# Optimization experiments

Hardware: AMD Instinct MI355X
Metric: run time of the kernel (lower is better)

The kernel has to match this reference:

```python
import jax, jax.numpy as jnp
import numpy as np

EPS_GN = 1e-8
EPS_ATTN = 1e-8


def setup_inputs() -> dict:
    key = jax.random.key(0)
    ks = jax.random.split(key, 13)
    B, C, N = 4, 512, 2048
    s = 0.02
    return {
        "x": jax.random.normal(ks[0], (B, C, N), jnp.float32),
        "dw_w": jax.random.normal(ks[1], (C, 3), jnp.float32) * s,
        "pw_w": jax.random.normal(ks[2], (C, C), jnp.float32) * s,
        "u_w": jax.random.normal(ks[3], (2 * C, C), jnp.float32) * s,
        "u_b": jax.random.normal(ks[4], (2 * C,), jnp.float32) * s,
        "v_w": jax.random.normal(ks[5], (2 * C, C), jnp.float32) * s,
        "v_b": jax.random.normal(ks[6], (2 * C,), jnp.float32) * s,
        "h_w": jax.random.normal(ks[7], (C, C), jnp.float32) * s,
        "h_b": jax.random.normal(ks[8], (C,), jnp.float32) * s,
        "q_w": jax.random.normal(ks[9], (C, C), jnp.float32) * s,
        "k_w": jax.random.normal(ks[10], (C, C), jnp.float32) * s,
        "o_w": jax.random.normal(ks[11], (C, 2 * C), jnp.float32) * s,
        "o_b": jax.random.normal(ks[12], (C,), jnp.float32) * s,
    }


def reference(x, dw_w, pw_w, u_w, u_b, v_w, v_b, h_w, h_b, q_w, k_w, o_w, o_b):
    # x: [B, C, N]
    C = x.shape[1]
    # GroupNorm(1, C): normalize over (C, N) per sample; affine is identity-init
    # in torch but we follow the module math with default weight=1, bias=0
    mean = jnp.mean(x, axis=(1, 2), keepdims=True)
    var = jnp.var(x, axis=(1, 2), keepdims=True)
    z = (x - mean) * jax.lax.rsqrt(var + EPS_GN)

    # local depthwise conv k=3, pad=1 (cross-correlation), no bias
    zp = jnp.pad(z, ((0, 0), (0, 0), (1, 1)))
    dw = (dw_w[:, 0, None] * zp[:, :, :-2]
          + dw_w[:, 1, None] * zp[:, :, 1:-1]
          + dw_w[:, 2, None] * zp[:, :, 2:])
    # pointwise conv (no bias)
    z = z + jnp.einsum('oc,bcn->bon', pw_w, dw)

    u = jax.nn.sigmoid(jnp.einsum('oc,bcn->bon', u_w, z) + u_b[:, None])  # [B,2C,N]
    v = jnp.einsum('oc,bcn->bon', v_w, z) + v_b[:, None]                  # [B,2C,N]
    h = jnp.einsum('oc,bcn->bno', h_w, z) + h_b                           # [B,N,C]

    q = h @ q_w.T  # [B,N,C]
    k = h @ k_w.T  # [B,N,C]
    scale = 1.0 / jnp.sqrt(jnp.float32(C))

    logits = jnp.einsum('bnc,bmc->bnm', q, k) * scale
    a = jax.nn.relu(logits)
    a = a * a
    a = a / (jnp.sum(a, axis=-1, keepdims=True) + EPS_ATTN)

    av = jnp.einsum('bnm,bom->bon', a, v)  # [B,2C,N]
    y = jnp.einsum('oc,bcn->bon', o_w, u * av) + o_b[:, None]
    return x + y
```

## Files before the change

kernel.cpp:

```cpp
#include <hip/hip_runtime.h>
#include <hip/hip_bf16.h>
#include <cstdint>

typedef __bf16 bhalf;
typedef __bf16 bhalf8 __attribute__((ext_vector_type(8)));
typedef float f32x4 __attribute__((ext_vector_type(4)));

enum { EPI_Z2=0, EPI_UV=1, EPI_BIAS=2, EPI_QK=3, EPI_ATTN=4, EPI_PV=5, EPI_Y=6 };

__device__ __forceinline__ void gl_lds16(const bhalf* g, bhalf* l) {
  __builtin_amdgcn_global_load_lds(
      (const __attribute__((address_space(1))) unsigned int*)g,
      (__attribute__((address_space(3))) unsigned int*)l,
      16, 0, 0);
}
__device__ __forceinline__ void barrier_raw() { asm volatile("s_barrier" ::: "memory"); }
#define VMW(n)  asm volatile("s_waitcnt vmcnt(" #n ")" ::: "memory")
#define LGKM0() asm volatile("s_waitcnt lgkmcnt(0)" ::: "memory")


template<int EPI>
__global__ void __launch_bounds__(512, 2)
gA(const bhalf* __restrict__ A, const bhalf* __restrict__ Bw,
   void* __restrict__ Out, void* __restrict__ Out2,
   const float* __restrict__ bias, const float* __restrict__ bias2,
   int N, int K, long sA, long sB, long sO, long sAuxf, float scale)
{
  constexpr int KSL = 256*64;
  constexpr int REG = 2*KSL;
  constexpr int DBUF = 2*REG;
  __shared__ __align__(16) char lds[2*DBUF];

  const int gx = gridDim.x, gy = gridDim.y;
  const int nwg = gx*gy;
  const int flat = blockIdx.y*gx + blockIdx.x;
  const int q8 = nwg>>3, r8 = nwg&7, xcd = flat&7, o8 = flat>>3;
  const int wsw = (xcd<r8 ? xcd*(q8+1) : r8*(q8+1)+(xcd-r8)*q8) + o8;
  const int bx = wsw % gx, by = wsw / gx;
  const int m0 = by*256, n0 = bx*256;
  const int bz = blockIdx.z;

  const bhalf* Ab = A + (long)bz*sA;
  const bhalf* Bb = Bw + (long)bz*sB;

  const int tid = threadIdx.x, wid = tid>>6, lane = tid&63;
  const int lm = lane&15, kq = lane>>4;
  const int wm = wid>>2, wn = wid&3;
  const int srow = lane>>2;
  const int csw = ((lane&3) ^ ((lane>>3)&3)) * 8;
  const int kqs = kq ^ ((lm>>1)&3);

  f32x4 acc[8][4];
  #pragma unroll
  for (int i=0;i<8;i++)
    #pragma unroll
    for (int j=0;j<4;j++) acc[i][j] = f32x4{0.f,0.f,0.f,0.f};

  auto stageA = [&](int kt){
    char* base = lds + (kt&1)*DBUF;
    const int k0 = kt*64;
    #pragma unroll
    for (int h=0; h<2; h++)
      #pragma unroll
      for (int ksl=0; ksl<2; ksl++){
        bhalf* d = (bhalf*)(base + ksl*KSL + (h*128 + wid*16)*64);
        gl_lds16(Ab + (long)(m0 + h*128 + wid*16 + srow)*K + k0 + ksl*32 + csw, d);
      }
  };
  auto stageB = [&](int kt){
    char* base = lds + (kt&1)*DBUF + REG;
    const int k0 = kt*64;
    #pragma unroll
    for (int h=0; h<2; h++)
      #pragma unroll
      for (int ksl=0; ksl<2; ksl++){
        bhalf* d = (bhalf*)(base + ksl*KSL + (h*128 + wid*16)*64);
        gl_lds16(Bb + (long)(n0 + h*128 + wid*16 + srow)*K + k0 + ksl*32 + csw, d);
      }
  };

  bhalf8 af[4][2], bf[4][2];
  auto readA = [&](int kt, int ih){
    char* base = lds + (kt&1)*DBUF;
    #pragma unroll
    for (int i2=0;i2<4;i2++)
      #pragma unroll
      for (int ksl=0;ksl<2;ksl++)
        af[i2][ksl] = *(const bhalf8*)(base + ksl*KSL + (wm*128 + ih*64 + i2*16 + lm)*64 + kqs*16);
  };
  auto readB = [&](int kt, int jh){
    char* base = lds + (kt&1)*DBUF + REG;
    #pragma unroll
    for (int j2=0;j2<2;j2++)
      #pragma unroll
      for (int ksl=0;ksl<2;ksl++)
        bf[jh*2+j2][ksl] = *(const bhalf8*)(base + ksl*KSL + (wn*64 + jh*32 + j2*16 + lm)*64 + kqs*16);
  };
  auto mfma16 = [&](int ih, int jh){
    __builtin_amdgcn_s_setprio(1);
    #pragma unroll
    for (int i2=0;i2<4;i2++)
      #pragma unroll
      for (int j2=0;j2<2;j2++)
        #pragma unroll
        for (int ksl=0;ksl<2;ksl++)
          acc[ih*4+i2][jh*2+j2] = __builtin_amdgcn_mfma_f32_16x16x32_bf16(
              af[i2][ksl], bf[jh*2+j2][ksl], acc[ih*4+i2][jh*2+j2], 0,0,0);
    __builtin_amdgcn_s_setprio(0);
  };

  const int NT = K>>6;
  stageA(0); stageB(0); stageA(1);
  for (int kt=0; kt<NT; ++kt){
    if (kt==NT-1) { VMW(0); } else { VMW(4); }
    barrier_raw();
    readA(kt,0); readB(kt,0);
    if (kt+1<NT) stageB(kt+1);
    mfma16(0,0);
    barrier_raw();
    readB(kt,1);
    mfma16(0,1);
    barrier_raw();
    readA(kt,1);
    mfma16(1,0);
    barrier_raw();
    if (kt+2<NT) stageA(kt+2);
    mfma16(1,1);
  }
  barrier_raw();

  char* obase; int ldb;
  const float* bv = nullptr; int bc0 = 0; bool sig = false;
  if constexpr (EPI==EPI_ATTN){
    obase = (char*)Out + 2*((long)bz*sO + (long)m0*N + n0); ldb = N*2;
  }
  if constexpr (EPI==EPI_UV){
    bool uh = n0 < 1024; sig = uh;
    obase = (char*)(uh?Out:Out2) + 2*((long)m0*1024 + (n0 - (uh?0:1024)));
    ldb = 2048; bv = uh ? bias : bias2; bc0 = uh ? n0 : n0-1024;
  }

  float rs[8][4];
  if constexpr (EPI==EPI_ATTN){
    #pragma unroll
    for (int i=0;i<8;i++)
      #pragma unroll
      for (int r=0;r<4;r++) rs[i][r]=0.f;
  }
  #pragma unroll
  for (int i=0;i<8;i++){
    #pragma unroll
    for (int j=0;j<4;j++){
      const int lcol = wn*64 + j*16 + lm;
      #pragma unroll
      for (int r=0;r<4;r++){
        const int lrow = wm*128 + i*16 + kq*4 + r;
        float v = acc[i][j][r];
        if constexpr (EPI==EPI_ATTN){
          v *= scale; v = fmaxf(v,0.f); v = v*v;
          rs[i][r] += v;
        }
        if constexpr (EPI==EPI_UV){
          v += bv[bc0 + lcol];
          if (sig) v = 1.f/(1.f + __expf(-v));
        }
        const int cb = lcol*2;
        const int lb = lrow*512 + (((cb>>5) ^ ((lrow>>2)&3))<<5) + (cb&31);
        *(bhalf*)(lds + lb) = (bhalf)v;
      }
    }
  }
  if constexpr (EPI==EPI_ATTN){
    float* rd = (float*)Out2;
    #pragma unroll
    for (int i=0;i<8;i++){
      const int rbase = m0 + wm*128 + i*16 + kq*4;
      #pragma unroll
      for (int r=0;r<4;r++){
        float s = rs[i][r];
        s += __shfl_xor(s,1); s += __shfl_xor(s,2);
        s += __shfl_xor(s,4); s += __shfl_xor(s,8);
        if (lm==0) atomicAdd(rd + (long)bz*sAuxf + rbase + r, s);
      }
    }
  }
  LGKM0();
  barrier_raw();
  #pragma unroll
  for (int it=0; it<16; ++it){
    const int g = (it*512 + tid)*16;
    const int row = g >> 9, off = g & 511;
    const int lb = row*512 + (((off>>5) ^ ((row>>2)&3))<<5) + (off&31);
    uint4 val = *(const uint4*)(lds + lb);
    *(uint4*)(obase + (long)row*ldb + off) = val;
  }
  (void)scale; (void)bias; (void)bias2; (void)N;
}

template<int EPI>
__global__ void __launch_bounds__(512, 2)
gB(const bhalf* __restrict__ A, const bhalf* __restrict__ Bw,
   void* __restrict__ Out, void* __restrict__ Out2,
   const bhalf* __restrict__ auxb, const float* __restrict__ auxf,
   int N, int K, long sB, float scale, int rowshift)
{
  constexpr int KSLA = 256*64;
  constexpr int KSLB = 128*64;
  constexpr int REGA = 2*KSLA;
  constexpr int DBUF = REGA + 2*KSLB;
  __shared__ __align__(16) char lds[3*DBUF];

  const int gx = gridDim.x, gy = gridDim.y;
  const int nwg = gx*gy;
  const int flat = blockIdx.y*gx + blockIdx.x;
  const int q8 = nwg>>3, r8 = nwg&7, xcd = flat&7, o8 = flat>>3;
  const int wsw = (xcd<r8 ? xcd*(q8+1) : r8*(q8+1)+(xcd-r8)*q8) + o8;
  const int bx = wsw % gx, by = wsw / gx;
  const int m0 = by*256, n0 = bx*128;

  const bhalf* Ab = A;
  const bhalf* Bb = Bw + (rowshift ? (long)(m0>>rowshift)*sB : 0);

  const int tid = threadIdx.x, wid = tid>>6, lane = tid&63;
  const int lm = lane&15, kq = lane>>4;
  const int wm = wid>>1, wn = wid&1;
  const int srow = lane>>2;
  const int csw = ((lane&3) ^ ((lane>>3)&3)) * 8;
  const int kqs = kq ^ ((lm>>1)&3);

  f32x4 acc[4][4];
  #pragma unroll
  for (int i=0;i<4;i++)
    #pragma unroll
    for (int j=0;j<4;j++) acc[i][j] = f32x4{0.f,0.f,0.f,0.f};

  auto stageAB = [&](int kt){
    char* base = lds + (kt%3)*DBUF;
    const int k0 = kt*64;
    #pragma unroll
    for (int h=0; h<2; h++)
      #pragma unroll
      for (int ksl=0; ksl<2; ksl++){
        bhalf* d = (bhalf*)(base + ksl*KSLA + (h*128 + wid*16)*64);
        gl_lds16(Ab + (long)(m0 + h*128 + wid*16 + srow)*K + k0 + ksl*32 + csw, d);
      }
    #pragma unroll
    for (int ksl=0; ksl<2; ksl++){
      bhalf* d = (bhalf*)(base + REGA + ksl*KSLB + (wid*16)*64);
      gl_lds16(Bb + (long)(n0 + wid*16 + srow)*K + k0 + ksl*32 + csw, d);
    }
  };

  bhalf8 af[4][2], bf[4][2];
  auto readA = [&](int kt){
    char* base = lds + (kt%3)*DBUF;
    #pragma unroll
    for (int i2=0;i2<4;i2++)
      #pragma unroll
      for (int ksl=0;ksl<2;ksl++)
        af[i2][ksl] = *(const bhalf8*)(base + ksl*KSLA + (wm*64 + i2*16 + lm)*64 + kqs*16);
  };
  auto readB = [&](int kt, int jh){
    char* base = lds + (kt%3)*DBUF + REGA;
    #pragma unroll
    for (int j2=0;j2<2;j2++)
      #pragma unroll
      for (int ksl=0;ksl<2;ksl++)
        bf[jh*2+j2][ksl] = *(const bhalf8*)(base + ksl*KSLB + (wn*64 + jh*32 + j2*16 + lm)*64 + kqs*16);
  };
  auto mfma16 = [&](int jh){
    __builtin_amdgcn_s_setprio(1);
    #pragma unroll
    for (int i2=0;i2<4;i2++)
      #pragma unroll
      for (int j2=0;j2<2;j2++)
        #pragma unroll
        for (int ksl=0;ksl<2;ksl++)
          acc[i2][jh*2+j2] = __builtin_amdgcn_mfma_f32_16x16x32_bf16(
              af[i2][ksl], bf[jh*2+j2][ksl], acc[i2][jh*2+j2], 0,0,0);
    __builtin_amdgcn_s_setprio(0);
  };

  const int NT = K>>6;
  stageAB(0); stageAB(1);
  for (int kt=0; kt<NT; ++kt){
    if (kt==NT-1) { VMW(0); } else { VMW(6); }
    barrier_raw();
    readA(kt); readB(kt,0);
    if (kt+2<NT) stageAB(kt+2);
    mfma16(0);
    barrier_raw();
    readB(kt,1);
    mfma16(1);
  }
  barrier_raw();

  char* obase; int ldb;
  if constexpr (EPI==EPI_PV){
    obase = (char*)Out + 2*((long)m0*1024 + n0); ldb = 2048;
  }
  if constexpr (EPI==EPI_QK){
    bool qh = n0 < 512;
    obase = (char*)(qh?Out:Out2) + 2*((long)m0*512 + (n0 - (qh?0:512)));
    ldb = 1024;
  }
  #pragma unroll
  for (int i=0;i<4;i++){
    #pragma unroll
    for (int j=0;j<4;j++){
      const int lcol = wn*64 + j*16 + lm;
      #pragma unroll
      for (int r=0;r<4;r++){
        const int lrow = wm*64 + i*16 + kq*4 + r;
        float v = acc[i][j][r];
        if constexpr (EPI==EPI_PV){
          const int rowg = m0 + lrow;
          float den = auxf[rowg];
          v *= __builtin_amdgcn_rcpf(den + 1e-8f);
          v *= (float)auxb[(long)rowg*1024 + n0 + lcol];
        }
        const int cb = lcol*2;
        const int lb = lrow*256 + (((cb>>5) ^ ((lrow>>2)&3))<<5) + (cb&31);
        *(bhalf*)(lds + lb) = (bhalf)v;
      }
    }
  }
  LGKM0();
  barrier_raw();
  #pragma unroll
  for (int it=0; it<8; ++it){
    const int g = (it*512 + tid)*16;
    const int row = g >> 8, off = g & 255;
    const int lb = row*256 + (((off>>5) ^ ((row>>2)&3))<<5) + (off&31);
    uint4 val = *(const uint4*)(lds + lb);
    *(uint4*)(obase + (long)row*ldb + off) = val;
  }
  (void)scale; (void)auxb; (void)auxf; (void)N;
}

template<int EPI>
__global__ void __launch_bounds__(512, 2)
gemm_bt(const bhalf* __restrict__ A, const bhalf* __restrict__ Bw,
        void* __restrict__ Out,
        const float* __restrict__ bias,
        const bhalf* __restrict__ auxb,
        int M, int N, int K)
{
  constexpr int STRIDE = 256*64;
  __shared__ __align__(16) char lds[4*STRIDE];

  const int gx = gridDim.x, gy = gridDim.y;
  const int nwg = gx*gy;
  const int flat = blockIdx.y*gx + blockIdx.x;
  const int q8 = nwg>>3, r8 = nwg&7, xcd = flat&7, o8 = flat>>3;
  const int w = (xcd<r8 ? xcd*(q8+1) : r8*(q8+1)+(xcd-r8)*q8) + o8;
  const int bx = w % gx, by = w / gx;

  const int tid = threadIdx.x;
  const int wid = tid>>6, lane = tid&63;
  const int lm = lane&15, kq = lane>>4;
  const int wm = wid>>2, wn = wid&3;
  const int m0 = by*128, n0 = bx*128;
  const int srow = lane>>2;
  const int csw = ((lane&3) ^ ((lane>>3)&3))*8;
  const int kqs = kq ^ ((lm>>1)&3);

  f32x4 acc[4][2];
  #pragma unroll
  for (int i=0;i<4;i++)
    #pragma unroll
    for (int j=0;j<2;j++) acc[i][j] = f32x4{0.f,0.f,0.f,0.f};

  auto stage = [&](int t){
    char* base = lds + (t&3)*STRIDE;
    const int k0 = t*32;
    #pragma unroll
    for (int c=0;c<2;c++){
      const int r0 = wid*32 + c*16;
      bhalf* d = (bhalf*)(base + r0*64);
      const bhalf* g = (r0 < 128)
        ? A + (long)(m0 + r0 + srow)*K + k0 + csw
        : Bw + (long)(n0 + r0 - 128 + srow)*K + k0 + csw;
      gl_lds16(g, d);
    }
  };

  auto compute = [&](int t){
    char* base = lds + (t&3)*STRIDE;
    bhalf8 af[4], bf[2];
    #pragma unroll
    for (int i=0;i<4;i++)
      af[i] = *(const bhalf8*)(base + (wm*64 + i*16 + lm)*64 + kqs*16);
    #pragma unroll
    for (int j=0;j<2;j++)
      bf[j] = *(const bhalf8*)(base + (128 + wn*32 + j*16 + lm)*64 + kqs*16);
    __builtin_amdgcn_s_setprio(1);
    #pragma unroll
    for (int i=0;i<4;i++)
      #pragma unroll
      for (int j=0;j<2;j++)
        acc[i][j] = __builtin_amdgcn_mfma_f32_16x16x32_bf16(af[i], bf[j], acc[i][j], 0,0,0);
    __builtin_amdgcn_s_setprio(0);
  };

  const int NT = K>>5;
  stage(0); stage(1); stage(2);
  for (int t=0; t<NT; ++t){
    if (t+3<NT){ stage(t+3); VMW(6); }
    else if (t+2<NT) { VMW(4); }
    else if (t+1<NT) { VMW(2); }
    else             { VMW(0); }
    barrier_raw();
    compute(t);
    barrier_raw();
  }

  char* obase = (char*)Out + 2*((long)m0*N + n0);
  const int ldb = N*2;
  #pragma unroll
  for (int i=0;i<4;i++){
    #pragma unroll
    for (int j=0;j<2;j++){
      const int lcol = wn*32 + j*16 + lm;
      #pragma unroll
      for (int r=0;r<4;r++){
        const int lrow = wm*64 + i*16 + kq*4 + r;
        float v = acc[i][j][r];
        if constexpr (EPI==EPI_Z2)
          v += (float)auxb[(long)(m0+lrow)*N + n0 + lcol];
        if constexpr (EPI==EPI_BIAS || EPI==EPI_Y)
          v += bias[n0 + lcol];
        const int cb = lcol*2;
        const int lb = lrow*256 + (((cb>>5) ^ ((lrow>>2)&3))<<5) + (cb&31);
        *(bhalf*)(lds + lb) = (bhalf)v;
      }
    }
  }
  LGKM0();
  barrier_raw();
  #pragma unroll
  for (int it=0; it<4; ++it){
    const int g = (it*512 + tid)*16;
    const int row = g >> 8, off = g & 255;
    const int lb = row*256 + (((off>>5) ^ ((row>>2)&3))<<5) + (off&31);
    uint4 val = *(const uint4*)(lds + lb);
    *(uint4*)(obase + (long)row*ldb + off) = val;
  }
  (void)M;
}

struct CvtArgs { const float* src[7]; bhalf* dst[7]; int n[7]; };
__global__ void cvt_multi(CvtArgs a) {
  int seg = blockIdx.y;
  int i = (blockIdx.x*256 + threadIdx.x)*4;
  if (i >= a.n[seg]) return;
  float4 f = *(const float4*)(a.src[seg] + i);
  bhalf* d = a.dst[seg] + i;
  d[0]=(bhalf)f.x; d[1]=(bhalf)f.y; d[2]=(bhalf)f.z; d[3]=(bhalf)f.w;
}

__global__ void gn_part(const float* __restrict__ x, float* __restrict__ ps, float* __restrict__ pss) {
  int b = blockIdx.y;
  const float* xb = x + (long)b*(512*2048);
  float s=0.f, ss=0.f;
  #pragma unroll
  for (int it=0; it<8; it++){
    int idx = ((it*128 + blockIdx.x)*256 + threadIdx.x)*4;
    float4 f = *(const float4*)(xb + idx);
    s  += f.x+f.y+f.z+f.w;
    ss += f.x*f.x+f.y*f.y+f.z*f.z+f.w*f.w;
  }
  for (int off=32; off; off>>=1){ s += __shfl_xor(s,off); ss += __shfl_xor(ss,off); }
  __shared__ float ls[4], lss[4];
  int wid = threadIdx.x>>6, lane = threadIdx.x&63;
  if (lane==0){ ls[wid]=s; lss[wid]=ss; }
  __syncthreads();
  if (threadIdx.x==0){
    s = ls[0]+ls[1]+ls[2]+ls[3]; ss = lss[0]+lss[1]+lss[2]+lss[3];
    ps[b*128 + blockIdx.x] = s; pss[b*128 + blockIdx.x] = ss;
  }
}

__global__ void gn_final(const float* __restrict__ ps, const float* __restrict__ pss,
                         float* __restrict__ stats) {
  int b = blockIdx.x;
  float s = ps[b*128 + threadIdx.x], ss = pss[b*128 + threadIdx.x];
  for (int off=32; off; off>>=1){ s += __shfl_xor(s,off); ss += __shfl_xor(ss,off); }
  __shared__ float l0[2], l1[2];
  int wid = threadIdx.x>>6, lane = threadIdx.x&63;
  if (lane==0){ l0[wid]=s; l1[wid]=ss; }
  __syncthreads();
  if (threadIdx.x==0){
    s = l0[0]+l0[1]; ss = l1[0]+l1[1];
    float mean = s*(1.f/1048576.f);
    float var  = ss*(1.f/1048576.f) - mean*mean;
    stats[b*2] = mean; stats[b*2+1] = rsqrtf(var + 1e-8f);
  }
}

__global__ void norm_dw_T(const float* __restrict__ x, const float* __restrict__ stats,
                          const float* __restrict__ dw_w,
                          bhalf* __restrict__ zT, bhalf* __restrict__ dwT) {
  int b = blockIdx.z, n0 = blockIdx.x*32, c0 = blockIdx.y*32;
  float mean = stats[b*2], rstd = stats[b*2+1];
  __shared__ float zs[32][35];
  int tx = threadIdx.x, ty = threadIdx.y;
  #pragma unroll
  for (int r=0;r<4;r++){
    int c = c0 + ty + r*8;
    for (int cc=tx; cc<34; cc+=32){
      int n = n0 - 1 + cc;
      float v = 0.f;
      if (n>=0 && n<2048) v = (x[((long)b*512 + c)*2048 + n] - mean)*rstd;
      zs[ty + r*8][cc] = v;
    }
  }
  __syncthreads();
  float w0 = dw_w[(c0+tx)*3+0], w1 = dw_w[(c0+tx)*3+1], w2 = dw_w[(c0+tx)*3+2];
  #pragma unroll
  for (int r=0;r<4;r++){
    int ln = ty + r*8;
    float z = zs[tx][ln+1];
    float d = w0*zs[tx][ln] + w1*zs[tx][ln+1] + w2*zs[tx][ln+2];
    long o = ((long)b*2048 + n0 + ln)*512 + c0 + tx;
    zT[o] = (bhalf)z; dwT[o] = (bhalf)d;
  }
}

__global__ void transpose_bf16(const bhalf* __restrict__ in, bhalf* __restrict__ out,
                               int R, int C) {
  __shared__ bhalf t[32][33];
  int r0 = blockIdx.x*32, c0 = blockIdx.y*32;
  long ib = (long)blockIdx.z*R*C;
  int tx = threadIdx.x, ty = threadIdx.y;
  #pragma unroll
  for (int r=0;r<4;r++)
    t[ty + r*8][tx] = in[ib + (long)(r0 + ty + r*8)*C + c0 + tx];
  __syncthreads();
  #pragma unroll
  for (int r=0;r<4;r++)
    out[ib + (long)(c0 + ty + r*8)*R + r0 + tx] = t[tx][ty + r*8];
}

__global__ void final_add(const float* __restrict__ x, const bhalf* __restrict__ yT,
                          float* __restrict__ out) {
  __shared__ float t[32][33];
  int n0 = blockIdx.x*32, c0 = blockIdx.y*32, b = blockIdx.z;
  int tx = threadIdx.x, ty = threadIdx.y;
  #pragma unroll
  for (int r=0;r<4;r++)
    t[ty + r*8][tx] = (float)yT[((long)b*2048 + n0 + ty + r*8)*512 + c0 + tx];
  __syncthreads();
  #pragma unroll
  for (int r=0;r<4;r++){
    long idx = ((long)b*512 + c0 + ty + r*8)*2048 + n0 + tx;
    out[idx] = x[idx] + t[tx][ty + r*8];
  }
}

extern "C" void kernel_launch(void* const* d_in, const int* in_sizes, int n_in,
                              void* d_out, int out_size, void* d_ws, size_t ws_size,
                              hipStream_t stream) {
  (void)in_sizes; (void)n_in; (void)out_size; (void)ws_size;
  const float* x    = (const float*)d_in[0];
  const float* dw_w = (const float*)d_in[1];
  const float* pw_w = (const float*)d_in[2];
  const float* u_w  = (const float*)d_in[3];
  const float* u_b  = (const float*)d_in[4];
  const float* v_w  = (const float*)d_in[5];
  const float* v_b  = (const float*)d_in[6];
  const float* h_w  = (const float*)d_in[7];
  const float* h_b  = (const float*)d_in[8];
  const float* q_w  = (const float*)d_in[9];
  const float* k_w  = (const float*)d_in[10];
  const float* o_w  = (const float*)d_in[11];
  const float* o_b  = (const float*)d_in[12];
  float* out = (float*)d_out;

  char* ws = (char*)d_ws;
  size_t off = 0;
  auto alloc = [&](size_t bytes) -> void* {
    void* p = ws + off; off = (off + bytes + 255) & ~(size_t)255; return p;
  };

  float* ps    = (float*)alloc(4*128*4);
  float* pss   = (float*)alloc(4*128*4);
  float* stats = (float*)alloc(4*2*4);
  float* rden  = (float*)alloc(4*2048*4);
  bhalf* wb_pw = (bhalf*)alloc(512*512*2);
  bhalf* wb_uv = (bhalf*)alloc((size_t)2048*512*2);
  bhalf* wb_h  = (bhalf*)alloc(512*512*2);
  bhalf* wb_qk = (bhalf*)alloc((size_t)1024*512*2);
  bhalf* wb_o  = (bhalf*)alloc((size_t)512*1024*2);
  const size_t ACT = (size_t)4*2048*512;
  bhalf* zT   = (bhalf*)alloc(ACT*2);
  bhalf* dwT  = (bhalf*)alloc(ACT*2);
  bhalf* z2T  = (bhalf*)alloc(ACT*2);
  bhalf* ub   = (bhalf*)alloc(ACT*2*2);
  bhalf* vT   = (bhalf*)alloc(ACT*2*2);
  bhalf* v_fm = (bhalf*)alloc(ACT*2*2);
  bhalf* hb   = (bhalf*)alloc(ACT*2);
  bhalf* wsc  = (bhalf*)alloc((size_t)4*2048*2048*2);
  bhalf* uav  = (bhalf*)alloc(ACT*2*2);
  bhalf* qb = zT;  bhalf* kb = dwT;  bhalf* yT = vT;

  hipMemsetAsync(rden, 0, 4*2048*4, stream);

  CvtArgs ca;
  ca.src[0]=pw_w; ca.dst[0]=wb_pw;           ca.n[0]=512*512;
  ca.src[1]=u_w;  ca.dst[1]=wb_uv;           ca.n[1]=1024*512;
  ca.src[2]=v_w;  ca.dst[2]=wb_uv+1024*512;  ca.n[2]=1024*512;
  ca.src[3]=h_w;  ca.dst[3]=wb_h;            ca.n[3]=512*512;
  ca.src[4]=q_w;  ca.dst[4]=wb_qk;           ca.n[4]=512*512;
  ca.src[5]=k_w;  ca.dst[5]=wb_qk+512*512;   ca.n[5]=512*512;
  ca.src[6]=o_w;  ca.dst[6]=wb_o;            ca.n[6]=512*1024;
  cvt_multi<<<dim3(512,7), 256, 0, stream>>>(ca);

  gn_part<<<dim3(128,4), 256, 0, stream>>>(x, ps, pss);
  gn_final<<<dim3(4), 128, 0, stream>>>(ps, pss, stats);

  norm_dw_T<<<dim3(64,16,4), dim3(32,8), 0, stream>>>(x, stats, dw_w, zT, dwT);

  const float iscl = 0.044194173824159216f;
  gemm_bt<EPI_Z2><<<dim3(4,64,1), 512, 0, stream>>>(dwT, wb_pw, z2T,
      nullptr, zT, 8192, 512, 512);
  gA<EPI_UV><<<dim3(8,32,1), 512, 0, stream>>>(z2T, wb_uv, ub, vT,
      u_b, v_b, 2048, 512, 0, 0, 0, 0, 0.f);
  gemm_bt<EPI_BIAS><<<dim3(4,64,1), 512, 0, stream>>>(z2T, wb_h, hb,
      h_b, nullptr, 8192, 512, 512);
  gB<EPI_QK><<<dim3(8,32,1), 512, 0, stream>>>(hb, wb_qk, qb, kb,
      nullptr, nullptr, 1024, 512, 0, 0.f, 0);
  transpose_bf16<<<dim3(64,32,4), dim3(32,8), 0, stream>>>(vT, v_fm, 2048, 1024);
  gA<EPI_ATTN><<<dim3(8,8,4), 512, 0, stream>>>(qb, kb, wsc, rden,
      nullptr, nullptr, 2048, 512,
      (long)2048*512, (long)2048*512, (long)2048*2048, 2048, iscl);
  gB<EPI_PV><<<dim3(8,32,1), 512, 0, stream>>>(wsc, v_fm, uav, nullptr,
      ub, rden, 1024, 2048, (long)1024*2048, 0.f, 11);
  gemm_bt<EPI_Y><<<dim3(4,64,1), 512, 0, stream>>>(uav, wb_o, yT,
      o_b, nullptr, 8192, 512, 1024);
  final_add<<<dim3(64,16,4), dim3(32,8), 0, stream>>>(x, yT, out);
}
```

Measured before the change: 192.3 us.

## Fuse v transpose and final residual add into GEMM epilogues; retile small GEMMs

The UV GEMM epilogue now writes the v half transposed through LDS straight into feature-major layout, which removes the separate transpose kernel. The output GEMM epilogue transposes in LDS, adds x and writes the fp32 result directly, which removes the final_add kernel and the yT buffer. The 128x128 GEMMs are rewritten as g4k with 256 threads, a 64-deep K step, double buffering and a 4x4 MFMA tile per wave. This saves two launches and two full activation round-trips through memory, at the cost of more complex epilogues and 8-byte scattered LDS reads in the transposed paths.

```diff
diff --git a/kernel.cpp b/kernel.cpp
--- a/kernel.cpp
+++ b/kernel.cpp
@@ -129,48 +129,29 @@
   }
   barrier_raw();
 
-  char* obase; int ldb;
-  const float* bv = nullptr; int bc0 = 0; bool sig = false;
   if constexpr (EPI==EPI_ATTN){
-    obase = (char*)Out + 2*((long)bz*sO + (long)m0*N + n0); ldb = N*2;
-  }
-  if constexpr (EPI==EPI_UV){
-    bool uh = n0 < 1024; sig = uh;
-    obase = (char*)(uh?Out:Out2) + 2*((long)m0*1024 + (n0 - (uh?0:1024)));
-    ldb = 2048; bv = uh ? bias : bias2; bc0 = uh ? n0 : n0-1024;
-  }
-
-  float rs[8][4];
-  if constexpr (EPI==EPI_ATTN){
+    float rs[8][4];
     #pragma unroll
     for (int i=0;i<8;i++)
       #pragma unroll
       for (int r=0;r<4;r++) rs[i][r]=0.f;
-  }
-  #pragma unroll
-  for (int i=0;i<8;i++){
-    #pragma unroll
-    for (int j=0;j<4;j++){
-      const int lcol = wn*64 + j*16 + lm;
-      #pragma unroll
-      for (int r=0;r<4;r++){
-        const int lrow = wm*128 + i*16 + kq*4 + r;
-        float v = acc[i][j][r];
-        if constexpr (EPI==EPI_ATTN){
+    #pragma unroll
+    for (int i=0;i<8;i++){
+      #pragma unroll
+      for (int j=0;j<4;j++){
+        const int lcol = wn*64 + j*16 + lm;
+        #pragma unroll
+        for (int r=0;r<4;r++){
+          const int lrow = wm*128 + i*16 + kq*4 + r;
+          float v = acc[i][j][r];
           v *= scale; v = fmaxf(v,0.f); v = v*v;
           rs[i][r] += v;
+          const int cb = lcol*2;
+          const int lb = lrow*512 + (((cb>>5) ^ ((lrow>>2)&3))<<5) + (cb&31);
+          *(bhalf*)(lds + lb) = (bhalf)v;
         }
-        if constexpr (EPI==EPI_UV){
-          v += bv[bc0 + lcol];
-          if (sig) v = 1.f/(1.f + __expf(-v));
-        }
-        const int cb = lcol*2;
-        const int lb = lrow*512 + (((cb>>5) ^ ((lrow>>2)&3))<<5) + (cb&31);
-        *(bhalf*)(lds + lb) = (bhalf)v;
-      }
-    }
-  }
-  if constexpr (EPI==EPI_ATTN){
+      }
+    }
     float* rd = (float*)Out2;
     #pragma unroll
     for (int i=0;i<8;i++){
@@ -183,16 +164,71 @@
         if (lm==0) atomicAdd(rd + (long)bz*sAuxf + rbase + r, s);
       }
     }
-  }
-  LGKM0();
-  barrier_raw();
-  #pragma unroll
-  for (int it=0; it<16; ++it){
-    const int g = (it*512 + tid)*16;
-    const int row = g >> 9, off = g & 511;
-    const int lb = row*512 + (((off>>5) ^ ((row>>2)&3))<<5) + (off&31);
-    uint4 val = *(const uint4*)(lds + lb);
-    *(uint4*)(obase + (long)row*ldb + off) = val;
+    LGKM0();
+    barrier_raw();
+    char* obase = (char*)Out + 2*((long)bz*sO + (long)m0*N + n0);
+    const int ldb = N*2;
+    #pragma unroll
+    for (int it=0; it<16; ++it){
+      const int g = (it*512 + tid)*16;
+      const int row = g >> 9, off = g & 511;
+      const int lb = row*512 + (((off>>5) ^ ((row>>2)&3))<<5) + (off&31);
+      uint4 val = *(const uint4*)(lds + lb);
+      *(uint4*)(obase + (long)row*ldb + off) = val;
+    }
+  }
+  if constexpr (EPI==EPI_UV){
+    const bool uh = n0 < 1024;
+    const float* bv = uh ? bias : bias2;
+    const int bc0 = uh ? n0 : n0-1024;
+    #pragma unroll
+    for (int i=0;i<8;i++){
+      #pragma unroll
+      for (int j=0;j<4;j++){
+        const int lcol = wn*64 + j*16 + lm;
+        #pragma unroll
+        for (int r=0;r<4;r++){
+          const int lrow = wm*128 + i*16 + kq*4 + r;
+          float v = acc[i][j][r] + bv[bc0 + lcol];
+          if (uh){
+            v = 1.f/(1.f + __expf(-v));
+            const int cb = lcol*2;
+            const int lb = lrow*512 + (((cb>>5) ^ ((lrow>>2)&3))<<5) + (cb&31);
+            *(bhalf*)(lds + lb) = (bhalf)v;
+          } else {
+            const int lb = lcol*512 + 2*(lrow ^ ((lcol&15)<<2));
+            *(bhalf*)(lds + lb) = (bhalf)v;
+          }
+        }
+      }
+    }
+    LGKM0();
+    barrier_raw();
+    if (uh){
+      char* obase = (char*)Out + 2*((long)m0*1024 + n0);
+      #pragma unroll
+      for (int it=0; it<16; ++it){
+        const int g = (it*512 + tid)*16;
+        const int row = g >> 9, off = g & 511;
+        const int lb = row*512 + (((off>>5) ^ ((row>>2)&3))<<5) + (off&31);
+        uint4 val = *(const uint4*)(lds + lb);
+        *(uint4*)(obase + (long)row*2048 + off) = val;
+      }
+    } else {
+      char* vb = (char*)Out2 + 2*((long)(m0>>11)*1024*2048 + (long)(n0-1024)*2048 + (m0 & 2047));
+      #pragma unroll
+      for (int it=0; it<16; ++it){
+        const int g = (it*512 + tid)*16;
+        const int row = g >> 9, off = g & 511;
+        const int t0 = off >> 1;
+        const int s = (row&15)<<2;
+        unsigned long long lo = *(const unsigned long long*)(lds + row*512 + 2*(t0^s));
+        unsigned long long hi = *(const unsigned long long*)(lds + row*512 + 2*((t0+4)^s));
+        char* dst = vb + (long)row*4096 + off;
+        ((unsigned long long*)dst)[0] = lo;
+        ((unsigned long long*)dst)[1] = hi;
+      }
+    }
   }
   (void)scale; (void)bias; (void)bias2; (void)N;
 }
@@ -339,15 +375,17 @@
 }
 
 template<int EPI>
-__global__ void __launch_bounds__(512, 2)
-gemm_bt(const bhalf* __restrict__ A, const bhalf* __restrict__ Bw,
-        void* __restrict__ Out,
-        const float* __restrict__ bias,
-        const bhalf* __restrict__ auxb,
-        int M, int N, int K)
+__global__ void __launch_bounds__(256, 2)
+g4k(const bhalf* __restrict__ A, const bhalf* __restrict__ Bw,
+    void* __restrict__ Out,
+    const float* __restrict__ bias,
+    const bhalf* __restrict__ auxb,
+    const float* __restrict__ xadd,
+    int M, int N, int K)
 {
-  constexpr int STRIDE = 256*64;
-  __shared__ __align__(16) char lds[4*STRIDE];
+  constexpr int KSL = 256*64;
+  constexpr int DBUF = 2*KSL;
+  __shared__ __align__(16) char lds[2*DBUF];
 
   const int gx = gridDim.x, gy = gridDim.y;
   const int nwg = gx*gy;
@@ -355,98 +393,147 @@
   const int q8 = nwg>>3, r8 = nwg&7, xcd = flat&7, o8 = flat>>3;
   const int w = (xcd<r8 ? xcd*(q8+1) : r8*(q8+1)+(xcd-r8)*q8) + o8;
   const int bx = w % gx, by = w / gx;
+  const int m0 = by*128, n0 = bx*128;
 
   const int tid = threadIdx.x;
   const int wid = tid>>6, lane = tid&63;
   const int lm = lane&15, kq = lane>>4;
-  const int wm = wid>>2, wn = wid&3;
-  const int m0 = by*128, n0 = bx*128;
+  const int wm = wid>>1, wn = wid&1;
   const int srow = lane>>2;
   const int csw = ((lane&3) ^ ((lane>>3)&3))*8;
   const int kqs = kq ^ ((lm>>1)&3);
 
-  f32x4 acc[4][2];
+  f32x4 acc[4][4];
   #pragma unroll
   for (int i=0;i<4;i++)
     #pragma unroll
-    for (int j=0;j<2;j++) acc[i][j] = f32x4{0.f,0.f,0.f,0.f};
-
-  auto stage = [&](int t){
-    char* base = lds + (t&3)*STRIDE;
-    const int k0 = t*32;
-    #pragma unroll
-    for (int c=0;c<2;c++){
-      const int r0 = wid*32 + c*16;
-      bhalf* d = (bhalf*)(base + r0*64);
-      const bhalf* g = (r0 < 128)
-        ? A + (long)(m0 + r0 + srow)*K + k0 + csw
-        : Bw + (long)(n0 + r0 - 128 + srow)*K + k0 + csw;
-      gl_lds16(g, d);
-    }
-  };
-
-  auto compute = [&](int t){
-    char* base = lds + (t&3)*STRIDE;
-    bhalf8 af[4], bf[2];
-    #pragma unroll
-    for (int i=0;i<4;i++)
-      af[i] = *(const bhalf8*)(base + (wm*64 + i*16 + lm)*64 + kqs*16);
-    #pragma unroll
-    for (int j=0;j<2;j++)
-      bf[j] = *(const bhalf8*)(base + (128 + wn*32 + j*16 + lm)*64 + kqs*16);
+    for (int j=0;j<4;j++) acc[i][j] = f32x4{0.f,0.f,0.f,0.f};
+
+  auto stage = [&](int kt){
+    char* base = lds + (kt&1)*DBUF;
+    const int k0 = kt*64;
+    #pragma unroll
+    for (int c=0;c<4;c++){
+      const int r0 = c*64 + wid*16;
+      #pragma unroll
+      for (int ksl=0; ksl<2; ksl++){
+        bhalf* d = (bhalf*)(base + ksl*KSL + r0*64);
+        const bhalf* g = (r0 < 128)
+          ? A  + (long)(m0 + r0 + srow)*K + k0 + ksl*32 + csw
+          : Bw + (long)(n0 + r0 - 128 + srow)*K + k0 + ksl*32 + csw;
+        gl_lds16(g, d);
+      }
+    }
+  };
+
+  bhalf8 af[4][2], bf[4][2];
+  auto readA = [&](int kt){
+    char* base = lds + (kt&1)*DBUF;
+    #pragma unroll
+    for (int i2=0;i2<4;i2++)
+      #pragma unroll
+      for (int ksl=0;ksl<2;ksl++)
+        af[i2][ksl] = *(const bhalf8*)(base + ksl*KSL + (wm*64 + i2*16 + lm)*64 + kqs*16);
+  };
+  auto readB = [&](int kt, int jh){
+    char* base = lds + (kt&1)*DBUF;
+    #pragma unroll
+    for (int j2=0;j2<2;j2++)
+      #pragma unroll
+      for (int ksl=0;ksl<2;ksl++)
+        bf[jh*2+j2][ksl] = *(const bhalf8*)(base + ksl*KSL + (128 + wn*64 + jh*32 + j2*16 + lm)*64 + kqs*16);
+  };
+  auto mfma16 = [&](int jh){
     __builtin_amdgcn_s_setprio(1);
     #pragma unroll
-    for (int i=0;i<4;i++)
-      #pragma unroll
-      for (int j=0;j<2;j++)
-        acc[i][j] = __builtin_amdgcn_mfma_f32_16x16x32_bf16(af[i], bf[j], acc[i][j], 0,0,0);
+    for (int i2=0;i2<4;i2++)
+      #pragma unroll
+      for (int j2=0;j2<2;j2++)
+        #pragma unroll
+        for (int ksl=0;ksl<2;ksl++)
+          acc[i2][jh*2+j2] = __builtin_amdgcn_mfma_f32_16x16x32_bf16(
+              af[i2][ksl], bf[jh*2+j2][ksl], acc[i2][jh*2+j2], 0,0,0);
     __builtin_amdgcn_s_setprio(0);
   };
 
-  const int NT = K>>5;
-  stage(0); stage(1); stage(2);
-  for (int t=0; t<NT; ++t){
-    if (t+3<NT){ stage(t+3); VMW(6); }
-    else if (t+2<NT) { VMW(4); }
-    else if (t+1<NT) { VMW(2); }
-    else             { VMW(0); }
-    barrier_raw();
-    compute(t);
-    barrier_raw();
-  }
-
-  char* obase = (char*)Out + 2*((long)m0*N + n0);
-  const int ldb = N*2;
-  #pragma unroll
-  for (int i=0;i<4;i++){
-    #pragma unroll
-    for (int j=0;j<2;j++){
-      const int lcol = wn*32 + j*16 + lm;
-      #pragma unroll
-      for (int r=0;r<4;r++){
-        const int lrow = wm*64 + i*16 + kq*4 + r;
-        float v = acc[i][j][r];
-        if constexpr (EPI==EPI_Z2)
-          v += (float)auxb[(long)(m0+lrow)*N + n0 + lcol];
-        if constexpr (EPI==EPI_BIAS || EPI==EPI_Y)
-          v += bias[n0 + lcol];
-        const int cb = lcol*2;
-        const int lb = lrow*256 + (((cb>>5) ^ ((lrow>>2)&3))<<5) + (cb&31);
-        *(bhalf*)(lds + lb) = (bhalf)v;
-      }
-    }
-  }
-  LGKM0();
+  const int NT = K>>6;
+  stage(0); stage(1);
+  for (int kt=0; kt<NT; ++kt){
+    if (kt==NT-1) { VMW(0); } else { VMW(8); }
+    barrier_raw();
+    readA(kt); readB(kt,0);
+    mfma16(0);
+    barrier_raw();
+    readB(kt,1);
+    if (kt+2<NT) stage(kt+2);
+    mfma16(1);
+  }
   barrier_raw();
-  #pragma unroll
-  for (int it=0; it<4; ++it){
-    const int g = (it*512 + tid)*16;
-    const int row = g >> 8, off = g & 255;
-    const int lb = row*256 + (((off>>5) ^ ((row>>2)&3))<<5) + (off&31);
-    uint4 val = *(const uint4*)(lds + lb);
-    *(uint4*)(obase + (long)row*ldb + off) = val;
-  }
-  (void)M;
+
+  if constexpr (EPI==EPI_Y){
+    #pragma unroll
+    for (int i=0;i<4;i++){
+      #pragma unroll
+      for (int j=0;j<4;j++){
+        const int lcol = wn*64 + j*16 + lm;
+        #pragma unroll
+        for (int r=0;r<4;r++){
+          const int lrow = wm*64 + i*16 + kq*4 + r;
+          float v = acc[i][j][r] + bias[n0 + lcol];
+          const int lb = lcol*512 + 4*(lrow ^ ((lcol&15)<<2));
+          *(float*)(lds + lb) = v;
+        }
+      }
+    }
+    LGKM0();
+    barrier_raw();
+    const int b = m0 >> 11, nb = m0 & 2047;
+    float* ob = (float*)Out + ((long)b*512 + n0)*2048 + nb;
+    const float* xb = xadd + ((long)b*512 + n0)*2048 + nb;
+    #pragma unroll
+    for (int it=0; it<16; ++it){
+      const int g = (it*256 + tid)*16;
+      const int row = g >> 9, off = g & 511;
+      const int t0 = off >> 2;
+      const int s = (row&15)<<2;
+      f32x4 vv = *(const f32x4*)(lds + row*512 + 4*(t0^s));
+      f32x4 xx = *(const f32x4*)(xb + (long)row*2048 + t0);
+      *(f32x4*)(ob + (long)row*2048 + t0) = vv + xx;
+    }
+  } else {
+    char* obase = (char*)Out + 2*((long)m0*N + n0);
+    const int ldb = N*2;
+    #pragma unroll
+    for (int i=0;i<4;i++){
+      #pragma unroll
+      for (int j=0;j<4;j++){
+        const int lcol = wn*64 + j*16 + lm;
+        #pragma unroll
+        for (int r=0;r<4;r++){
+          const int lrow = wm*64 + i*16 + kq*4 + r;
+          float v = acc[i][j][r];
+          if constexpr (EPI==EPI_Z2)
+            v += (float)auxb[(long)(m0+lrow)*N + n0 + lcol];
+          if constexpr (EPI==EPI_BIAS)
+            v += bias[n0 + lcol];
+          const int cb = lcol*2;
+          const int lb = lrow*256 + (((cb>>5) ^ ((lrow>>2)&3))<<5) + (cb&31);
+          *(bhalf*)(lds + lb) = (bhalf)v;
+        }
+      }
+    }
+    LGKM0();
+    barrier_raw();
+    #pragma unroll
+    for (int it=0; it<8; ++it){
+      const int g = (it*256 + tid)*16;
+      const int row = g >> 8, off = g & 255;
+      const int lb = row*256 + (((off>>5) ^ ((row>>2)&3))<<5) + (off&31);
+      uint4 val = *(const uint4*)(lds + lb);
+      *(uint4*)(obase + (long)row*ldb + off) = val;
+    }
+  }
+  (void)M; (void)xadd; (void)bias; (void)auxb;
 }
 
 struct CvtArgs { const float* src[7]; bhalf* dst[7]; int n[7]; };
@@ -524,37 +611,6 @@
     float d = w0*zs[tx][ln] + w1*zs[tx][ln+1] + w2*zs[tx][ln+2];
     long o = ((long)b*2048 + n0 + ln)*512 + c0 + tx;
     zT[o] = (bhalf)z; dwT[o] = (bhalf)d;
-  }
-}
-
-__global__ void transpose_bf16(const bhalf* __restrict__ in, bhalf* __restrict__ out,
-                               int R, int C) {
-  __shared__ bhalf t[32][33];
-  int r0 = blockIdx.x*32, c0 = blockIdx.y*32;
-  long ib = (long)blockIdx.z*R*C;
-  int tx = threadIdx.x, ty = threadIdx.y;
-  #pragma unroll
-  for (int r=0;r<4;r++)
-    t[ty + r*8][tx] = in[ib + (long)(r0 + ty + r*8)*C + c0 + tx];
-  __syncthreads();
-  #pragma unroll
-  for (int r=0;r<4;r++)
-    out[ib + (long)(c0 + ty + r*8)*R + r0 + tx] = t[tx][ty + r*8];
-}
-
-__global__ void final_add(const float* __restrict__ x, const bhalf* __restrict__ yT,
-                          float* __restrict__ out) {
-  __shared__ float t[32][33];
-  int n0 = blockIdx.x*32, c0 = blockIdx.y*32, b = blockIdx.z;
-  int tx = threadIdx.x, ty = threadIdx.y;
-  #pragma unroll
-  for (int r=0;r<4;r++)
-    t[ty + r*8][tx] = (float)yT[((long)b*2048 + n0 + ty + r*8)*512 + c0 + tx];
-  __syncthreads();
-  #pragma unroll
-  for (int r=0;r<4;r++){
-    long idx = ((long)b*512 + c0 + ty + r*8)*2048 + n0 + tx;
-    out[idx] = x[idx] + t[tx][ty + r*8];
   }
 }
 
@@ -597,12 +653,11 @@
   bhalf* dwT  = (bhalf*)alloc(ACT*2);
   bhalf* z2T  = (bhalf*)alloc(ACT*2);
   bhalf* ub   = (bhalf*)alloc(ACT*2*2);
-  bhalf* vT   = (bhalf*)alloc(ACT*2*2);
   bhalf* v_fm = (bhalf*)alloc(ACT*2*2);
   bhalf* hb   = (bhalf*)alloc(ACT*2);
   bhalf* wsc  = (bhalf*)alloc((size_t)4*2048*2048*2);
   bhalf* uav  = (bhalf*)alloc(ACT*2*2);
-  bhalf* qb = zT;  bhalf* kb = dwT;  bhalf* yT = vT;
+  bhalf* qb = zT;  bhalf* kb = dwT;
 
   hipMemsetAsync(rden, 0, 4*2048*4, stream);
 
@@ -622,21 +677,19 @@
   norm_dw_T<<<dim3(64,16,4), dim3(32,8), 0, stream>>>(x, stats, dw_w, zT, dwT);
 
   const float iscl = 0.044194173824159216f;
-  gemm_bt<EPI_Z2><<<dim3(4,64,1), 512, 0, stream>>>(dwT, wb_pw, z2T,
-      nullptr, zT, 8192, 512, 512);
-  gA<EPI_UV><<<dim3(8,32,1), 512, 0, stream>>>(z2T, wb_uv, ub, vT,
+  g4k<EPI_Z2><<<dim3(4,64,1), 256, 0, stream>>>(dwT, wb_pw, z2T,
+      nullptr, zT, nullptr, 8192, 512, 512);
+  gA<EPI_UV><<<dim3(8,32,1), 512, 0, stream>>>(z2T, wb_uv, ub, v_fm,
       u_b, v_b, 2048, 512, 0, 0, 0, 0, 0.f);
-  gemm_bt<EPI_BIAS><<<dim3(4,64,1), 512, 0, stream>>>(z2T, wb_h, hb,
-      h_b, nullptr, 8192, 512, 512);
+  g4k<EPI_BIAS><<<dim3(4,64,1), 256, 0, stream>>>(z2T, wb_h, hb,
+      h_b, nullptr, nullptr, 8192, 512, 512);
   gB<EPI_QK><<<dim3(8,32,1), 512, 0, stream>>>(hb, wb_qk, qb, kb,
       nullptr, nullptr, 1024, 512, 0, 0.f, 0);
-  transpose_bf16<<<dim3(64,32,4), dim3(32,8), 0, stream>>>(vT, v_fm, 2048, 1024);
   gA<EPI_ATTN><<<dim3(8,8,4), 512, 0, stream>>>(qb, kb, wsc, rden,
       nullptr, nullptr, 2048, 512,
       (long)2048*512, (long)2048*512, (long)2048*2048, 2048, iscl);
   gB<EPI_PV><<<dim3(8,32,1), 512, 0, stream>>>(wsc, v_fm, uav, nullptr,
       ub, rden, 1024, 2048, (long)1024*2048, 0.f, 11);
-  gemm_bt<EPI_Y><<<dim3(4,64,1), 512, 0, stream>>>(uav, wb_o, yT,
-      o_b, nullptr, 8192, 512, 1024);
-  final_add<<<dim3(64,16,4), dim3(32,8), 0, stream>>>(x, yT, out);
-}
+  g4k<EPI_Y><<<dim3(4,64,1), 256, 0, stream>>>(uav, wb_o, out,
+      o_b, nullptr, x, 8192, 512, 1024);
+}
```

New measurement: 183.7 us. 1.05x faster.
